# Performance work log

Measured on AMD Instinct MI355X. Metric: run time of the kernel, lower is better.

Reference implementation:

```python
import jax, jax.numpy as jnp
import numpy as np

B, N, DIM, HEADS = 8, 1024, 512, 8
HEAD_DIM = DIM // HEADS
SCALE = HEAD_DIM ** -0.5
NEG_BIG = -1.0e12


def setup_inputs() -> dict:
    key = jax.random.key(0)
    k_x, k_qw, k_qb, k_pw, k_pb = jax.random.split(key, 5)
    # torch nn.Linear layout: weight [out, in], y = x @ W.T + b
    s_qkv = (DIM) ** -0.5
    return {
        "x": jax.random.normal(k_x, (B, N, DIM), dtype=jnp.float32),
        "qkv_w": jax.random.uniform(k_qw, (3 * DIM, DIM), minval=-s_qkv, maxval=s_qkv, dtype=jnp.float32),
        "qkv_b": jax.random.uniform(k_qb, (3 * DIM,), minval=-s_qkv, maxval=s_qkv, dtype=jnp.float32),
        "proj_w": jax.random.uniform(k_pw, (DIM, DIM), minval=-s_qkv, maxval=s_qkv, dtype=jnp.float32),
        "proj_b": jax.random.uniform(k_pb, (DIM,), minval=-s_qkv, maxval=s_qkv, dtype=jnp.float32),
    }


def reference(x, qkv_w, qkv_b, proj_w, proj_b):
    b, n, c = x.shape
    qkv = x @ qkv_w.T + qkv_b                      # [B, N, 3*C]
    qkv = qkv.reshape(b, n, 3, HEADS, c // HEADS)
    qkv = jnp.transpose(qkv, (2, 0, 3, 1, 4))      # [3, B, H, N, hd]
    q, k, v = qkv[0], qkv[1], qkv[2]
    attn = jnp.einsum("bhqd,bhkd->bhqk", q, k) * SCALE  # [B, H, N, N]
    # bernoulli(p=0.5) mask added as -1e12 bias (deterministic key)
    mask = jax.random.bernoulli(jax.random.key(42), 0.5, attn.shape)
    attn = attn + mask.astype(attn.dtype) * NEG_BIG
    attn = jax.nn.softmax(attn, axis=-1)
    # dropout p=0.0 -> identity
    out = jnp.einsum("bhqk,bhkd->bhqd", attn, v)   # [B, H, N, hd]
    out = jnp.transpose(out, (0, 2, 1, 3)).reshape(b, n, c)
    return out @ proj_w.T + proj_b
```

## Files before the change

kernel.cpp:

```cpp
#include <hip/hip_runtime.h>
#include <stdint.h>

typedef uint32_t u32;
using bf16x8 = __attribute__((ext_vector_type(8))) short;
using f32x4  = __attribute__((ext_vector_type(4))) float;

#define MFMA16(a, b, c) __builtin_amdgcn_mfma_f32_16x16x32_bf16((a), (b), (c), 0, 0, 0)

__device__ __forceinline__ unsigned short f2bf(float f) {
  u32 u = __builtin_bit_cast(u32, f);
  return (unsigned short)((u + 0x7FFFu + ((u >> 16) & 1u)) >> 16);
}

__device__ __forceinline__ void gl_lds16(const unsigned short* g, unsigned short* l) {
  __builtin_amdgcn_global_load_lds((const __attribute__((address_space(1))) void*)g,
                                   (__attribute__((address_space(3))) void*)l, 16, 0, 0);
}

#define TFR(r) x0 += x1; x1 = (x1 << (r)) | (x1 >> (32 - (r))); x1 ^= x0;

__device__ __forceinline__ void threefry2x32(u32 i0, u32 i1, u32& o0, u32& o1) {
  const u32 ks0 = 0u, ks1 = 42u, ks2 = 0x1BD11BDAu ^ 42u;
  u32 x0 = i0 + ks0;
  u32 x1 = i1 + ks1;
  TFR(13) TFR(15) TFR(26) TFR(6)
  x0 += ks1; x1 += ks2 + 1u;
  TFR(17) TFR(29) TFR(16) TFR(24)
  x0 += ks2; x1 += ks0 + 2u;
  TFR(13) TFR(15) TFR(26) TFR(6)
  x0 += ks0; x1 += ks1 + 3u;
  TFR(17) TFR(29) TFR(16) TFR(24)
  x0 += ks1; x1 += ks2 + 4u;
  TFR(13) TFR(15) TFR(26) TFR(6)
  x0 += ks2; x1 += ks0 + 5u;
  o0 = x0; o1 = x1;
}

__device__ __forceinline__ u32 keep_bit(u32 j) {
  u32 o0, o1;
  threefry2x32(0u, j, o0, o1);
  return (o0 ^ o1) >> 31;
}

__global__ __launch_bounds__(256) void cvt_kernel(
    const float* __restrict__ x, const float* __restrict__ qw, const float* __restrict__ pw,
    unsigned short* __restrict__ xb, unsigned short* __restrict__ qwb,
    unsigned short* __restrict__ pwb) {
  int t = blockIdx.x * 256 + threadIdx.x;
  const float4* src; unsigned short* dst; int idx;
  if (t < 1048576)      { src = (const float4*)x;  dst = xb;  idx = t; }
  else if (t < 1245184) { src = (const float4*)qw; dst = qwb; idx = t - 1048576; }
  else                  { src = (const float4*)pw; dst = pwb; idx = t - 1245184; }
  float4 v = src[idx];
  ushort4 o = make_ushort4(f2bf(v.x), f2bf(v.y), f2bf(v.z), f2bf(v.w));
  ((ushort4*)dst)[idx] = o;
}

template<int EPI>
__global__ __launch_bounds__(256)
void gemm_kernel(const unsigned short* __restrict__ A, const unsigned short* __restrict__ Bm,
                 const float* __restrict__ bias, unsigned short* __restrict__ q_out,
                 unsigned short* __restrict__ k_out, unsigned short* __restrict__ vt_out,
                 float* __restrict__ f_out) {
  __shared__ __align__(16) unsigned short lA[128 * 32];
  __shared__ __align__(16) unsigned short lB[128 * 32];
  const int tid = threadIdx.x;
  const int lane = tid & 63, w = tid >> 6;
  const int hi = lane >> 4, lo = lane & 15;
  const int wm = w >> 1, wn = w & 1;
  const int m0 = blockIdx.y * 128, n0 = blockIdx.x * 128;
  const int srow = lane >> 2, skc = (lane & 3) * 8;

  f32x4 acc[4][4];
#pragma unroll
  for (int i = 0; i < 4; ++i)
#pragma unroll
    for (int j = 0; j < 4; ++j) acc[i][j] = (f32x4){0.f, 0.f, 0.f, 0.f};

  for (int kt = 0; kt < 16; ++kt) {
    const int k0 = kt * 32;
    __syncthreads();
#pragma unroll
    for (int c = 0; c < 2; ++c) {
      const int rr = (w * 2 + c) * 16 + srow;
      gl_lds16(A  + (size_t)(m0 + rr) * 512 + k0 + skc, &lA[(w * 2 + c) * 512]);
      gl_lds16(Bm + (size_t)(n0 + rr) * 512 + k0 + skc, &lB[(w * 2 + c) * 512]);
    }
    __syncthreads();

    bf16x8 af[4], bfr[4];
#pragma unroll
    for (int i = 0; i < 4; ++i) af[i]  = *(const bf16x8*)&lA[(wm * 64 + i * 16 + lo) * 32 + hi * 8];
#pragma unroll
    for (int i = 0; i < 4; ++i) bfr[i] = *(const bf16x8*)&lB[(wn * 64 + i * 16 + lo) * 32 + hi * 8];
#pragma unroll
    for (int i = 0; i < 4; ++i)
#pragma unroll
      for (int j = 0; j < 4; ++j)
        acc[i][j] = MFMA16(af[i], bfr[j], acc[i][j]);
  }

#pragma unroll
  for (int i = 0; i < 4; ++i) {
    const int rowb = m0 + wm * 64 + i * 16 + hi * 4;
#pragma unroll
    for (int j = 0; j < 4; ++j) {
      const int col = n0 + wn * 64 + j * 16 + lo;
      const float bv = bias[col];
      if (EPI == 0) {
        const int which = col >> 9, hh = (col >> 6) & 7, dd = col & 63;
#pragma unroll
        for (int r = 0; r < 4; ++r) {
          const int tok = rowb + r;
          const int b = tok >> 10, nt = tok & 1023;
          const int bh = b * 8 + hh;
          const unsigned short val = f2bf(acc[i][j][r] + bv);
          if (which == 0)      q_out[((size_t)((bh << 10) + nt)) * 64 + dd] = val;
          else if (which == 1) k_out[((size_t)((bh << 10) + nt)) * 64 + dd] = val;
          else                 vt_out[((size_t)bh * 64 + dd) * 1024 + nt] = val;
        }
      } else {
#pragma unroll
        for (int r = 0; r < 4; ++r)
          f_out[(size_t)(rowb + r) * 512 + col] = acc[i][j][r] + bv;
      }
    }
  }
}

__global__ __launch_bounds__(256) void attn_kernel(
    const unsigned short* __restrict__ Qb, const unsigned short* __restrict__ Kb,
    const unsigned short* __restrict__ VTb, unsigned short* __restrict__ aout) {
  __shared__ __align__(16) unsigned short plds[4][16 * 40];
  const int tid = threadIdx.x;
  const int lane = tid & 63, w = tid >> 6;
  const int hi = lane >> 4, lo = lane & 15;
  const int bid = blockIdx.x;
  const int qt = bid & 15, bh = bid >> 4;
  const int qs = qt * 64 + w * 16;

  bf16x8 qf[2];
#pragma unroll
  for (int dh = 0; dh < 2; ++dh)
    qf[dh] = *(const bf16x8*)&Qb[((size_t)(bh << 10) + qs + lo) * 64 + dh * 32 + hi * 8];

  f32x4 acc[4];
  f32x4 sacc = (f32x4){0.f, 0.f, 0.f, 0.f};
  float mrun[4];
#pragma unroll
  for (int dt = 0; dt < 4; ++dt) acc[dt] = (f32x4){0.f, 0.f, 0.f, 0.f};
#pragma unroll
  for (int r = 0; r < 4; ++r) mrun[r] = -1e30f;
  bf16x8 ones;
#pragma unroll
  for (int j = 0; j < 8; ++j) ones[j] = (short)0x3F80;

  for (int kt = 0; kt < 32; ++kt) {
    const int k0 = kt * 32;

    u32 keep[2][4];
#pragma unroll
    for (int t = 0; t < 2; ++t)
#pragma unroll
      for (int r = 0; r < 4; ++r) {
        const u32 j = ((u32)bh << 20) | ((u32)(qs + hi * 4 + r) << 10) | (u32)(k0 + t * 16 + lo);
        keep[t][r] = keep_bit(j);
      }

    f32x4 st[2];
#pragma unroll
    for (int t = 0; t < 2; ++t) {
      const unsigned short* kbp = &Kb[((size_t)(bh << 10) + k0 + t * 16 + lo) * 64 + hi * 8];
      bf16x8 kf0 = *(const bf16x8*)kbp;
      bf16x8 kf1 = *(const bf16x8*)(kbp + 32);
      f32x4 z = (f32x4){0.f, 0.f, 0.f, 0.f};
      z = MFMA16(qf[0], kf0, z);
      z = MFMA16(qf[1], kf1, z);
      st[t] = z;
    }
    float sc[2][4];
#pragma unroll
    for (int t = 0; t < 2; ++t)
#pragma unroll
      for (int r = 0; r < 4; ++r)
        sc[t][r] = keep[t][r] ? st[t][r] * 0.125f : -1e30f;

    float tm[4];
#pragma unroll
    for (int r = 0; r < 4; ++r) tm[r] = fmaxf(sc[0][r], sc[1][r]);
#pragma unroll
    for (int d = 1; d < 16; d <<= 1)
#pragma unroll
      for (int r = 0; r < 4; ++r) tm[r] = fmaxf(tm[r], __shfl_xor(tm[r], d));

    float ps[4];
#pragma unroll
    for (int r = 0; r < 4; ++r) {
      const float nm = fmaxf(mrun[r], tm[r]);
      ps[r] = __expf(mrun[r] - nm);
      mrun[r] = nm;
    }
#pragma unroll
    for (int dt = 0; dt < 4; ++dt)
#pragma unroll
      for (int r = 0; r < 4; ++r) acc[dt][r] *= ps[r];
#pragma unroll
    for (int r = 0; r < 4; ++r) sacc[r] *= ps[r];

    unsigned short* mp = &plds[w][0];
#pragma unroll
    for (int t = 0; t < 2; ++t)
#pragma unroll
      for (int r = 0; r < 4; ++r) {
        const float p = keep[t][r] ? __expf(sc[t][r] - mrun[r]) : 0.f;
        mp[(hi * 4 + r) * 40 + t * 16 + lo] = f2bf(p);
      }

    asm volatile("s_waitcnt lgkmcnt(0)" ::: "memory");

    bf16x8 pf = *(const bf16x8*)&mp[lo * 40 + hi * 8];
    sacc = MFMA16(pf, ones, sacc);
#pragma unroll
    for (int dt = 0; dt < 4; ++dt) {
      bf16x8 vf = *(const bf16x8*)&VTb[((size_t)(bh * 64 + dt * 16 + lo)) * 1024 + k0 + hi * 8];
      acc[dt] = MFMA16(pf, vf, acc[dt]);
    }
    asm volatile("s_waitcnt lgkmcnt(0)" ::: "memory");
  }

  const int b = bh >> 3, h = bh & 7;
#pragma unroll
  for (int r = 0; r < 4; ++r) {
    const float inv = 1.0f / sacc[r];
    const int tok = (b << 10) + qs + hi * 4 + r;
#pragma unroll
    for (int dt = 0; dt < 4; ++dt)
      aout[(size_t)tok * 512 + h * 64 + dt * 16 + lo] = f2bf(acc[dt][r] * inv);
  }
}

extern "C" void kernel_launch(void* const* d_in, const int* in_sizes, int n_in,
                              void* d_out, int out_size, void* d_ws, size_t ws_size,
                              hipStream_t stream) {
  const float* x      = (const float*)d_in[0];
  const float* qkv_w  = (const float*)d_in[1];
  const float* qkv_b  = (const float*)d_in[2];
  const float* proj_w = (const float*)d_in[3];
  const float* proj_b = (const float*)d_in[4];
  float* out = (float*)d_out;
  char* ws = (char*)d_ws;

  unsigned short* xb  = (unsigned short*)(ws);
  unsigned short* qwb = (unsigned short*)(ws +  8388608);
  unsigned short* pwb = (unsigned short*)(ws +  9961472);
  unsigned short* Qb  = (unsigned short*)(ws + 10485760);
  unsigned short* Kb  = (unsigned short*)(ws + 18874368);
  unsigned short* VTb = (unsigned short*)(ws + 27262976);

  cvt_kernel<<<5120, 256, 0, stream>>>(x, qkv_w, proj_w, xb, qwb, pwb);
  gemm_kernel<0><<<dim3(12, 64), 256, 0, stream>>>(xb, qwb, qkv_b, Qb, Kb, VTb, nullptr);
  attn_kernel<<<1024, 256, 0, stream>>>(Qb, Kb, VTb, xb);
  gemm_kernel<1><<<dim3(4, 64), 256, 0, stream>>>(xb, pwb, proj_b, nullptr, nullptr, nullptr, out);
}
```

Measured before the change: 249.1 us.

## Widen attention key tile to 64, fold softmax scale into Q, cheapen threefry

The attention loop now processes 64 keys per iteration instead of 32, issuing two PV MFMAs per V tile and using a wider padded LDS buffer for P. The 1/sqrt(d) scale is folded into the Q projection epilogue, so the per-score multiply disappears. The threefry mask hash is specialised with constant-folded zero keys and uses alignbit rotates. The launch bounds now ask for occupancy 4, and the trailing LDS wait and the masked-p select are dropped. The aim is less per-iteration overhead and fewer ALU ops in the RNG-heavy loop, at the cost of more registers per iteration.

```diff
diff --git a/kernel.cpp b/kernel.cpp
--- a/kernel.cpp
+++ b/kernel.cpp
@@ -17,29 +17,26 @@
                                    (__attribute__((address_space(3))) void*)l, 16, 0, 0);
 }
 
-#define TFR(r) x0 += x1; x1 = (x1 << (r)) | (x1 >> (32 - (r))); x1 ^= x0;
-
-__device__ __forceinline__ void threefry2x32(u32 i0, u32 i1, u32& o0, u32& o1) {
-  const u32 ks0 = 0u, ks1 = 42u, ks2 = 0x1BD11BDAu ^ 42u;
-  u32 x0 = i0 + ks0;
-  u32 x1 = i1 + ks1;
+__device__ __forceinline__ u32 rotl(u32 x, int r) {
+  return __builtin_amdgcn_alignbit(x, x, 32 - r);
+}
+#define TFR(r) x0 += x1; x1 = rotl(x1, r) ^ x0;
+
+__device__ __forceinline__ u32 keep_bit(u32 j) {
+  const u32 ks1 = 42u, ks2 = 0x1BD11BDAu ^ 42u;
+  u32 x0 = 0u;
+  u32 x1 = j + ks1;
   TFR(13) TFR(15) TFR(26) TFR(6)
   x0 += ks1; x1 += ks2 + 1u;
   TFR(17) TFR(29) TFR(16) TFR(24)
-  x0 += ks2; x1 += ks0 + 2u;
+  x0 += ks2; x1 += 0u + 2u;
   TFR(13) TFR(15) TFR(26) TFR(6)
-  x0 += ks0; x1 += ks1 + 3u;
+  x0 += 0u; x1 += ks1 + 3u;
   TFR(17) TFR(29) TFR(16) TFR(24)
   x0 += ks1; x1 += ks2 + 4u;
   TFR(13) TFR(15) TFR(26) TFR(6)
-  x0 += ks2; x1 += ks0 + 5u;
-  o0 = x0; o1 = x1;
-}
-
-__device__ __forceinline__ u32 keep_bit(u32 j) {
-  u32 o0, o1;
-  threefry2x32(0u, j, o0, o1);
-  return (o0 ^ o1) >> 31;
+  x0 += ks2; x1 += 0u + 5u;
+  return (x0 ^ x1) >> 31;
 }
 
 __global__ __launch_bounds__(256) void cvt_kernel(
@@ -109,12 +106,13 @@
       const float bv = bias[col];
       if (EPI == 0) {
         const int which = col >> 9, hh = (col >> 6) & 7, dd = col & 63;
+        const float scl = (which == 0) ? 0.125f : 1.0f;
 #pragma unroll
         for (int r = 0; r < 4; ++r) {
           const int tok = rowb + r;
           const int b = tok >> 10, nt = tok & 1023;
           const int bh = b * 8 + hh;
-          const unsigned short val = f2bf(acc[i][j][r] + bv);
+          const unsigned short val = f2bf((acc[i][j][r] + bv) * scl);
           if (which == 0)      q_out[((size_t)((bh << 10) + nt)) * 64 + dd] = val;
           else if (which == 1) k_out[((size_t)((bh << 10) + nt)) * 64 + dd] = val;
           else                 vt_out[((size_t)bh * 64 + dd) * 1024 + nt] = val;
@@ -128,10 +126,10 @@
   }
 }
 
-__global__ __launch_bounds__(256) void attn_kernel(
+__global__ __launch_bounds__(256, 4) void attn_kernel(
     const unsigned short* __restrict__ Qb, const unsigned short* __restrict__ Kb,
     const unsigned short* __restrict__ VTb, unsigned short* __restrict__ aout) {
-  __shared__ __align__(16) unsigned short plds[4][16 * 40];
+  __shared__ __align__(16) unsigned short plds[4][16 * 68];
   const int tid = threadIdx.x;
   const int lane = tid & 63, w = tid >> 6;
   const int hi = lane >> 4, lo = lane & 15;
@@ -155,39 +153,35 @@
 #pragma unroll
   for (int j = 0; j < 8; ++j) ones[j] = (short)0x3F80;
 
-  for (int kt = 0; kt < 32; ++kt) {
-    const int k0 = kt * 32;
-
-    u32 keep[2][4];
-#pragma unroll
-    for (int t = 0; t < 2; ++t)
-#pragma unroll
-      for (int r = 0; r < 4; ++r) {
-        const u32 j = ((u32)bh << 20) | ((u32)(qs + hi * 4 + r) << 10) | (u32)(k0 + t * 16 + lo);
-        keep[t][r] = keep_bit(j);
-      }
-
-    f32x4 st[2];
-#pragma unroll
-    for (int t = 0; t < 2; ++t) {
+  const u32 jbase = ((u32)bh << 20) | ((u32)(qs + hi * 4) << 10) | (u32)lo;
+
+  for (int kt = 0; kt < 16; ++kt) {
+    const int k0 = kt * 64;
+
+    u32 keep[4][4];
+#pragma unroll
+    for (int t = 0; t < 4; ++t)
+#pragma unroll
+      for (int r = 0; r < 4; ++r)
+        keep[t][r] = keep_bit(jbase + ((u32)r << 10) + (u32)(k0 + t * 16));
+
+    float sc[4][4];
+#pragma unroll
+    for (int t = 0; t < 4; ++t) {
       const unsigned short* kbp = &Kb[((size_t)(bh << 10) + k0 + t * 16 + lo) * 64 + hi * 8];
       bf16x8 kf0 = *(const bf16x8*)kbp;
       bf16x8 kf1 = *(const bf16x8*)(kbp + 32);
       f32x4 z = (f32x4){0.f, 0.f, 0.f, 0.f};
       z = MFMA16(qf[0], kf0, z);
       z = MFMA16(qf[1], kf1, z);
-      st[t] = z;
-    }
-    float sc[2][4];
-#pragma unroll
-    for (int t = 0; t < 2; ++t)
-#pragma unroll
-      for (int r = 0; r < 4; ++r)
-        sc[t][r] = keep[t][r] ? st[t][r] * 0.125f : -1e30f;
+#pragma unroll
+      for (int r = 0; r < 4; ++r) sc[t][r] = keep[t][r] ? z[r] : -1e30f;
+    }
 
     float tm[4];
 #pragma unroll
-    for (int r = 0; r < 4; ++r) tm[r] = fmaxf(sc[0][r], sc[1][r]);
+    for (int r = 0; r < 4; ++r)
+      tm[r] = fmaxf(fmaxf(sc[0][r], sc[1][r]), fmaxf(sc[2][r], sc[3][r]));
 #pragma unroll
     for (int d = 1; d < 16; d <<= 1)
 #pragma unroll
@@ -209,23 +203,25 @@
 
     unsigned short* mp = &plds[w][0];
 #pragma unroll
-    for (int t = 0; t < 2; ++t)
-#pragma unroll
-      for (int r = 0; r < 4; ++r) {
-        const float p = keep[t][r] ? __expf(sc[t][r] - mrun[r]) : 0.f;
-        mp[(hi * 4 + r) * 40 + t * 16 + lo] = f2bf(p);
-      }
+    for (int t = 0; t < 4; ++t)
+#pragma unroll
+      for (int r = 0; r < 4; ++r)
+        mp[(hi * 4 + r) * 68 + t * 16 + lo] = f2bf(__expf(sc[t][r] - mrun[r]));
 
     asm volatile("s_waitcnt lgkmcnt(0)" ::: "memory");
 
-    bf16x8 pf = *(const bf16x8*)&mp[lo * 40 + hi * 8];
-    sacc = MFMA16(pf, ones, sacc);
+    bf16x8 pf[2];
+#pragma unroll
+    for (int ks = 0; ks < 2; ++ks)
+      pf[ks] = *(const bf16x8*)&mp[lo * 68 + ks * 32 + hi * 8];
+    sacc = MFMA16(pf[0], ones, sacc);
+    sacc = MFMA16(pf[1], ones, sacc);
 #pragma unroll
     for (int dt = 0; dt < 4; ++dt) {
-      bf16x8 vf = *(const bf16x8*)&VTb[((size_t)(bh * 64 + dt * 16 + lo)) * 1024 + k0 + hi * 8];
-      acc[dt] = MFMA16(pf, vf, acc[dt]);
-    }
-    asm volatile("s_waitcnt lgkmcnt(0)" ::: "memory");
+      const unsigned short* vbp = &VTb[((size_t)(bh * 64 + dt * 16 + lo)) * 1024 + k0 + hi * 8];
+      acc[dt] = MFMA16(pf[0], *(const bf16x8*)vbp, acc[dt]);
+      acc[dt] = MFMA16(pf[1], *(const bf16x8*)(vbp + 32), acc[dt]);
+    }
   }
 
   const int b = bh >> 3, h = bh & 7;
```

After: 210.9 us. 15.3% less time.
